# Kernel optimization log

Measured on AMD Instinct MI355X. Metric: run time of the kernel, lower is better.

The kernel has to match this reference:

```python
import jax, jax.numpy as jnp
import numpy as np

B, S, HID = 2, 2048, 4096
NUM_HEADS, NUM_KV_HEADS, HEAD_DIM = 32, 8, 128
KV_SIZE = HID * NUM_KV_HEADS // NUM_HEADS  # 1024


def setup_inputs() -> dict:
    key = jax.random.key(0)
    ks = jax.random.split(key, 5)
    x = jax.random.normal(ks[0], (B, S, HID), dtype=jnp.float32)
    wq = jax.random.normal(ks[1], (HID, HID), dtype=jnp.float32) * 0.02
    wk = jax.random.normal(ks[2], (HID, KV_SIZE), dtype=jnp.float32) * 0.02
    wv = jax.random.normal(ks[3], (HID, KV_SIZE), dtype=jnp.float32) * 0.02
    wo = jax.random.normal(ks[4], (KV_SIZE, HID), dtype=jnp.float32) * 0.02
    return {"x": x, "wq": wq, "wk": wk, "wv": wv, "wo": wo}


def reference(x, wq, wk, wv, wo):
    b, s, _ = x.shape
    g = NUM_HEADS // NUM_KV_HEADS  # num_head_groups
    q = x @ wq  # [b, s, hid]
    k = x @ wk  # [b, s, kv_size]
    v = x @ wv  # [b, s, kv_size]
    # 'b s (h d) -> b h s d' with h = num_heads
    q = q.reshape(b, s, NUM_HEADS, HEAD_DIM).transpose(0, 2, 1, 3)
    # 'b s (h d) -> b h d s' with h = num_kv_heads
    k = k.reshape(b, s, NUM_KV_HEADS, HEAD_DIM).transpose(0, 2, 3, 1)
    # 'b s (h d) -> b h s d'
    v = v.reshape(b, s, NUM_KV_HEADS, HEAD_DIM).transpose(0, 2, 1, 3)
    # 'b (h g) s d -> b g h s d' with g = num_head_groups, h = num_kv_heads
    q = q.reshape(b, NUM_KV_HEADS, g, s, HEAD_DIM).transpose(0, 2, 1, 3, 4)
    # NOTE: faithful to source - g is contracted (summed) here, it does not
    # appear in the output subscripts.
    scores = jnp.einsum('bghqd,bhdk->bhqk', q, k) / jnp.sqrt(
        jnp.asarray(HEAD_DIM, dtype=x.dtype))
    scores = jax.nn.softmax(scores, axis=-1)
    values = jnp.einsum('bhqk,bhkd->bhqd', scores, v)  # [b, h_kv, s, d]
    values = values.transpose(0, 2, 1, 3).reshape(b, s, KV_SIZE)
    return values @ wo  # [b, s, hid]
```

## Files before the change

kernel.cpp:

```cpp
#include <hip/hip_runtime.h>
#include <stdint.h>

#define S 2048
#define HID 4096
#define NKV 8
#define HD 128
#define KV 1024
#define BATCH 2
#define NQKV 3072
#define MROWS 4096

typedef __attribute__((ext_vector_type(4))) float f32x4;
typedef __attribute__((ext_vector_type(8))) __bf16 bf16x8;
typedef __attribute__((ext_vector_type(8))) unsigned short ushort8;
typedef __attribute__((ext_vector_type(4))) unsigned short ushort4_t;
typedef __attribute__((ext_vector_type(4))) float float4_t;

__device__ __forceinline__ unsigned short f2bf(float f) {
    unsigned int u = __builtin_bit_cast(unsigned int, f);
    u += 0x7fffu + ((u >> 16) & 1u);
    return (unsigned short)(u >> 16);
}
__device__ __forceinline__ float bf2f(unsigned short s) {
    unsigned int u = ((unsigned int)s) << 16;
    return __builtin_bit_cast(float, u);
}

__device__ __forceinline__ void gl2lds16(const void* g, void* l) {
    __builtin_amdgcn_global_load_lds(
        (const __attribute__((address_space(1))) void*)(uintptr_t)(g),
        (__attribute__((address_space(3))) void*)(uintptr_t)(l),
        16, 0, 0);
}

__global__ __launch_bounds__(256) void castx_kernel(const float* __restrict__ x,
                                                    unsigned short* __restrict__ xb) {
    int i = (blockIdx.x * 256 + threadIdx.x) * 4;
    float4_t v = *(const float4_t*)&x[i];
    ushort4_t o;
    o.x = f2bf(v.x); o.y = f2bf(v.y); o.z = f2bf(v.z); o.w = f2bf(v.w);
    *(ushort4_t*)&xb[i] = o;
}

__global__ __launch_bounds__(256) void wcat_kernel(const float* __restrict__ wq,
                                                   const float* __restrict__ wk,
                                                   const float* __restrict__ wv,
                                                   unsigned short* __restrict__ WcatT) {
    __shared__ float T[64 * 65];
    const int tid = threadIdx.x;
    const int k0 = blockIdx.x * 64;
    const int n0 = blockIdx.y * 64;
    const float scale = 0.088388347648318447f;
#pragma unroll
    for (int i = 0; i < 16; i++) {
        int kl = (tid >> 6) + i * 4;
        int nl = tid & 63;
        int k = k0 + kl, n = n0 + nl;
        float v;
        if (n < KV) {
            int kvh = n >> 7, d = n & 127;
            const float* p = wq + (size_t)k * HID + kvh * 512 + d;
            v = (p[0] + p[128] + p[256] + p[384]) * scale;
        } else if (n < 2048) {
            v = wk[(size_t)k * KV + (n - KV)];
        } else {
            v = wv[(size_t)k * KV + (n - 2048)];
        }
        T[kl * 65 + nl] = v;
    }
    __syncthreads();
#pragma unroll
    for (int i = 0; i < 16; i++) {
        int nl = (tid >> 6) + i * 4;
        int kl = tid & 63;
        WcatT[(size_t)(n0 + nl) * HID + k0 + kl] = f2bf(T[kl * 65 + nl]);
    }
}

__global__ __launch_bounds__(256) void wot_kernel(const float* __restrict__ wo,
                                                  unsigned short* __restrict__ woT) {
    __shared__ float T[64 * 65];
    const int tid = threadIdx.x;
    const int k0 = blockIdx.x * 64;
    const int n0 = blockIdx.y * 64;
#pragma unroll
    for (int i = 0; i < 16; i++) {
        int kl = (tid >> 6) + i * 4, nl = tid & 63;
        T[kl * 65 + nl] = wo[(size_t)(k0 + kl) * HID + n0 + nl];
    }
    __syncthreads();
#pragma unroll
    for (int i = 0; i < 16; i++) {
        int nl = (tid >> 6) + i * 4, kl = tid & 63;
        woT[(size_t)(n0 + nl) * KV + k0 + kl] = f2bf(T[kl * 65 + nl]);
    }
}

template <int OUT_BF16>
__global__ __launch_bounds__(256) void gemm_bt(const unsigned short* __restrict__ A,
                                               const unsigned short* __restrict__ Bt,
                                               void* __restrict__ Cv,
                                               int M, int N, int K) {
    __shared__ unsigned short Asl[128 * 32];
    __shared__ unsigned short Bsl[128 * 32];
    const int tid = threadIdx.x;
    const int lane = tid & 63;
    const int wave = tid >> 6;
    const int lm = lane & 15;
    const int quad = lane >> 4;
    const int wm = (wave >> 1) << 6;
    const int wn = (wave & 1) << 6;
    const int m0 = blockIdx.y * 128;
    const int n0 = blockIdx.x * 128;

    f32x4 acc[4][4] = {};

    const int r0 = tid >> 2;
    const int kc = tid & 3;
    const int gsw = kc ^ ((r0 >> 1) & 3);
    const int rsw = (lm >> 1) & 3;
    const size_t Abase = (size_t)(m0 + r0) * K + gsw * 8;
    const size_t Bbase = (size_t)(n0 + r0) * K + gsw * 8;
    unsigned short* As0 = &Asl[tid * 8];
    unsigned short* As1 = &Asl[(tid + 256) * 8];
    unsigned short* Bs0 = &Bsl[tid * 8];
    unsigned short* Bs1 = &Bsl[(tid + 256) * 8];

    for (int k0 = 0; k0 < K; k0 += 32) {
        gl2lds16(A + Abase + k0, As0);
        gl2lds16(A + Abase + (size_t)64 * K + k0, As1);
        gl2lds16(Bt + Bbase + k0, Bs0);
        gl2lds16(Bt + Bbase + (size_t)64 * K + k0, Bs1);
        __syncthreads();
        bf16x8 af[4], bfr[4];
#pragma unroll
        for (int i = 0; i < 4; i++)
            af[i] = *(const bf16x8*)&Asl[(wm + i * 16 + lm) * 32 + (quad ^ rsw) * 8];
#pragma unroll
        for (int j = 0; j < 4; j++)
            bfr[j] = *(const bf16x8*)&Bsl[(wn + j * 16 + lm) * 32 + (quad ^ rsw) * 8];
#pragma unroll
        for (int i = 0; i < 4; i++)
#pragma unroll
            for (int j = 0; j < 4; j++)
                acc[i][j] = __builtin_amdgcn_mfma_f32_16x16x32_bf16(af[i], bfr[j], acc[i][j], 0, 0, 0);
        __syncthreads();
    }
#pragma unroll
    for (int i = 0; i < 4; i++) {
        const int row = m0 + wm + i * 16 + quad * 4;
#pragma unroll
        for (int j = 0; j < 4; j++) {
            const int col = n0 + wn + j * 16 + lm;
#pragma unroll
            for (int r = 0; r < 4; r++) {
                if (OUT_BF16)
                    ((unsigned short*)Cv)[(size_t)(row + r) * N + col] = f2bf(acc[i][j][r]);
                else
                    ((float*)Cv)[(size_t)(row + r) * N + col] = acc[i][j][r];
            }
        }
    }
}

__global__ __launch_bounds__(256) void vt_kernel(const unsigned short* __restrict__ QKV,
                                                 unsigned short* __restrict__ Vt) {
    __shared__ unsigned short T[128 * 136];
    const int tid = threadIdx.x;
    const int st = blockIdx.x;
    const int bh = blockIdx.y;
    const int b = bh >> 3, h = bh & 7;
#pragma unroll
    for (int it = 0; it < 8; it++) {
        int chunk = tid + it * 256;
        int s = chunk >> 4, cc = chunk & 15;
        ushort8 v = *(const ushort8*)&QKV[(size_t)(b * S + st * 128 + s) * NQKV + 2048 + h * HD + cc * 8];
        *(ushort8*)&T[s * 136 + cc * 8] = v;
    }
    __syncthreads();
#pragma unroll
    for (int it = 0; it < 8; it++) {
        int chunk = tid + it * 256;
        int d = chunk >> 4, scc = chunk & 15;
        ushort8 o;
#pragma unroll
        for (int j = 0; j < 8; j++) o[j] = T[(scc * 8 + j) * 136 + d];
        *(ushort8*)&Vt[(size_t)((b * NKV + h) * HD + d) * S + st * 128 + scc * 8] = o;
    }
}

__global__ __launch_bounds__(256, 1) void attn_kernel(const unsigned short* __restrict__ QKV,
                                                      const unsigned short* __restrict__ Vt,
                                                      unsigned short* __restrict__ Oout) {
    __shared__ unsigned short Ks[64 * 128];
    __shared__ unsigned short Vs[128 * 64];
    __shared__ unsigned short Ps[128 * 64];
    const int tid = threadIdx.x;
    const int lane = tid & 63, wave = tid >> 6;
    const int lm = lane & 15, quad = lane >> 4;
    const int sw = lm & 7;
    const int qt = blockIdx.x;
    const int h = blockIdx.y;
    const int b = blockIdx.z;
    const int qrow0 = qt * 128 + wave * 32;

    bf16x8 qf[2][4];
#pragma unroll
    for (int rt = 0; rt < 2; rt++)
#pragma unroll
        for (int ks = 0; ks < 4; ks++) {
            size_t off = (size_t)(b * S + qrow0 + rt * 16 + lm) * NQKV + h * HD + ks * 32 + quad * 8;
            qf[rt][ks] = *(const bf16x8*)&QKV[off];
        }

    float lsum[2][4] = {};
    f32x4 oacc[2][8] = {};

    const int krow = tid >> 2, kc4 = tid & 3;
    const int vrow = tid >> 1, vc2 = tid & 1;
    const unsigned short* Kg0 = QKV + (size_t)(b * S) * NQKV + KV + h * HD + kc4 * 32;
    const unsigned short* Vg0 = Vt + (size_t)((b * NKV + h) * HD + vrow) * S + vc2 * 32;

    ushort8 kreg[4], vreg[4];
    {
        const unsigned short* kg = Kg0 + (size_t)krow * NQKV;
        const unsigned short* vg = Vg0;
#pragma unroll
        for (int j = 0; j < 4; j++) kreg[j] = *(const ushort8*)(kg + j * 8);
#pragma unroll
        for (int j = 0; j < 4; j++) vreg[j] = *(const ushort8*)(vg + j * 8);
    }

    for (int kt = 0; kt < 32; kt++) {
        __syncthreads();
#pragma unroll
        for (int j = 0; j < 4; j++)
            *(ushort8*)&Ks[krow * 128 + ((kc4 * 4 + j) ^ (krow & 7)) * 8] = kreg[j];
#pragma unroll
        for (int j = 0; j < 4; j++)
            *(ushort8*)&Vs[vrow * 64 + ((vc2 * 4 + j) ^ (vrow & 7)) * 8] = vreg[j];
        __syncthreads();
        if (kt < 31) {
            const unsigned short* kg = Kg0 + (size_t)((kt + 1) * 64 + krow) * NQKV;
            const unsigned short* vg = Vg0 + (kt + 1) * 64;
#pragma unroll
            for (int j = 0; j < 4; j++) kreg[j] = *(const ushort8*)(kg + j * 8);
#pragma unroll
            for (int j = 0; j < 4; j++) vreg[j] = *(const ushort8*)(vg + j * 8);
        }

        f32x4 sc[2][4] = {};
#pragma unroll
        for (int ks = 0; ks < 4; ks++)
#pragma unroll
            for (int ct = 0; ct < 4; ct++) {
                bf16x8 kf = *(const bf16x8*)&Ks[(ct * 16 + lm) * 128 + ((ks * 4 + quad) ^ sw) * 8];
                sc[0][ct] = __builtin_amdgcn_mfma_f32_16x16x32_bf16(qf[0][ks], kf, sc[0][ct], 0, 0, 0);
                sc[1][ct] = __builtin_amdgcn_mfma_f32_16x16x32_bf16(qf[1][ks], kf, sc[1][ct], 0, 0, 0);
            }

#pragma unroll
        for (int rt = 0; rt < 2; rt++)
#pragma unroll
            for (int ct = 0; ct < 4; ct++)
#pragma unroll
                for (int r = 0; r < 4; r++) {
                    float p = __expf(fminf(sc[rt][ct][r], 60.f));
                    unsigned short pb = f2bf(p);
                    lsum[rt][r] += bf2f(pb);
                    int prow = wave * 32 + rt * 16 + quad * 4 + r;
                    int pcol = ct * 16 + lm;
                    Ps[prow * 64 + (((pcol >> 3) ^ (prow & 7)) * 8) + (pcol & 7)] = pb;
                }

#pragma unroll
        for (int ks = 0; ks < 2; ks++) {
            bf16x8 af0 = *(const bf16x8*)&Ps[(wave * 32 + lm) * 64 + ((ks * 4 + quad) ^ sw) * 8];
            bf16x8 af1 = *(const bf16x8*)&Ps[(wave * 32 + 16 + lm) * 64 + ((ks * 4 + quad) ^ sw) * 8];
#pragma unroll
            for (int dt = 0; dt < 8; dt++) {
                bf16x8 vf = *(const bf16x8*)&Vs[(dt * 16 + lm) * 64 + ((ks * 4 + quad) ^ sw) * 8];
                oacc[0][dt] = __builtin_amdgcn_mfma_f32_16x16x32_bf16(af0, vf, oacc[0][dt], 0, 0, 0);
                oacc[1][dt] = __builtin_amdgcn_mfma_f32_16x16x32_bf16(af1, vf, oacc[1][dt], 0, 0, 0);
            }
        }
    }

#pragma unroll
    for (int rt = 0; rt < 2; rt++)
#pragma unroll
        for (int r = 0; r < 4; r++) {
            float v = lsum[rt][r];
            v += __shfl_xor(v, 8);
            v += __shfl_xor(v, 4);
            v += __shfl_xor(v, 2);
            v += __shfl_xor(v, 1);
            lsum[rt][r] = v;
        }
#pragma unroll
    for (int rt = 0; rt < 2; rt++)
#pragma unroll
        for (int dt = 0; dt < 8; dt++)
#pragma unroll
            for (int r = 0; r < 4; r++) {
                int row = b * S + qt * 128 + wave * 32 + rt * 16 + quad * 4 + r;
                int col = h * HD + dt * 16 + lm;
                Oout[(size_t)row * KV + col] = f2bf(oacc[rt][dt][r] / lsum[rt][r]);
            }
}

extern "C" void kernel_launch(void* const* d_in, const int* in_sizes, int n_in,
                              void* d_out, int out_size, void* d_ws, size_t ws_size,
                              hipStream_t stream) {
    (void)in_sizes; (void)n_in; (void)out_size; (void)ws_size;
    const float* x  = (const float*)d_in[0];
    const float* wq = (const float*)d_in[1];
    const float* wk = (const float*)d_in[2];
    const float* wv = (const float*)d_in[3];
    const float* wo = (const float*)d_in[4];
    float* out = (float*)d_out;
    char* ws = (char*)d_ws;

    unsigned short* xb    = (unsigned short*)(ws);
    unsigned short* WcatT = (unsigned short*)(ws + 33554432);
    unsigned short* woT   = (unsigned short*)(ws + 33554432 + 25165824);
    unsigned short* QKV   = (unsigned short*)(ws + 67108864);
    unsigned short* Vt    = (unsigned short*)(ws);
    unsigned short* AttnO = (unsigned short*)(ws + 8388608);

    castx_kernel<<<16384, 256, 0, stream>>>(x, xb);
    wcat_kernel<<<dim3(64, 48), 256, 0, stream>>>(wq, wk, wv, WcatT);
    wot_kernel<<<dim3(16, 64), 256, 0, stream>>>(wo, woT);
    gemm_bt<1><<<dim3(NQKV / 128, MROWS / 128), 256, 0, stream>>>(xb, WcatT, QKV, MROWS, NQKV, HID);
    vt_kernel<<<dim3(16, 16), 256, 0, stream>>>(QKV, Vt);
    attn_kernel<<<dim3(16, NKV, BATCH), 256, 0, stream>>>(QKV, Vt, AttnO);
    gemm_bt<0><<<dim3(HID / 128, MROWS / 128), 256, 0, stream>>>(AttnO, woT, out, MROWS, HID, KV);
}
```

Baseline: 455.9 us.

## Replace GEMM with 256x256 tiled, double-buffered, 8-wave pipelined kernel

Replaces the simple 128x128 single-buffered bf16 GEMM with a 512-thread kernel that computes 256x256 tiles over 64-wide K steps. Global-to-LDS loads for the next K tile are double-buffered and interleaved with MFMA quarters, separated by barriers and explicit vmcnt waits, with s_setprio raised around the MFMA blocks. It also swizzles the LDS layout and remaps block IDs across 8 groups for better cache locality. The goal is to hide memory latency and raise data reuse, at the cost of much higher LDS and register use (two blocks per CU) and fewer blocks for these matrix sizes.

```diff
diff --git a/kernel.cpp b/kernel.cpp
--- a/kernel.cpp
+++ b/kernel.cpp
@@ -96,71 +96,150 @@
     }
 }
 
+#define BAR() do { asm volatile("" ::: "memory"); __builtin_amdgcn_s_barrier(); asm volatile("" ::: "memory"); } while (0)
+#define WAITV2() asm volatile("s_waitcnt vmcnt(2)" ::: "memory")
+
+__device__ __forceinline__ void stage2(const unsigned short* __restrict__ g,
+                                       size_t so0, size_t so1,
+                                       unsigned short* lds, int tid) {
+    gl2lds16(g + so0, lds + (size_t)tid * 8);
+    gl2lds16(g + so1, lds + (size_t)(512 + tid) * 8);
+}
+
 template <int OUT_BF16>
-__global__ __launch_bounds__(256) void gemm_bt(const unsigned short* __restrict__ A,
-                                               const unsigned short* __restrict__ Bt,
-                                               void* __restrict__ Cv,
-                                               int M, int N, int K) {
-    __shared__ unsigned short Asl[128 * 32];
-    __shared__ unsigned short Bsl[128 * 32];
+__global__ __launch_bounds__(512, 2) void gemm_bt8(const unsigned short* __restrict__ A,
+                                                   const unsigned short* __restrict__ Bt,
+                                                   void* __restrict__ Cv,
+                                                   int M, int N, int K) {
+    __shared__ unsigned short As[2][2][8192];
+    __shared__ unsigned short Bs[2][2][8192];
     const int tid = threadIdx.x;
-    const int lane = tid & 63;
-    const int wave = tid >> 6;
-    const int lm = lane & 15;
-    const int quad = lane >> 4;
-    const int wm = (wave >> 1) << 6;
-    const int wn = (wave & 1) << 6;
-    const int m0 = blockIdx.y * 128;
-    const int n0 = blockIdx.x * 128;
-
-    f32x4 acc[4][4] = {};
-
-    const int r0 = tid >> 2;
-    const int kc = tid & 3;
-    const int gsw = kc ^ ((r0 >> 1) & 3);
-    const int rsw = (lm >> 1) & 3;
-    const size_t Abase = (size_t)(m0 + r0) * K + gsw * 8;
-    const size_t Bbase = (size_t)(n0 + r0) * K + gsw * 8;
-    unsigned short* As0 = &Asl[tid * 8];
-    unsigned short* As1 = &Asl[(tid + 256) * 8];
-    unsigned short* Bs0 = &Bsl[tid * 8];
-    unsigned short* Bs1 = &Bsl[(tid + 256) * 8];
-
-    for (int k0 = 0; k0 < K; k0 += 32) {
-        gl2lds16(A + Abase + k0, As0);
-        gl2lds16(A + Abase + (size_t)64 * K + k0, As1);
-        gl2lds16(Bt + Bbase + k0, Bs0);
-        gl2lds16(Bt + Bbase + (size_t)64 * K + k0, Bs1);
-        __syncthreads();
-        bf16x8 af[4], bfr[4];
-#pragma unroll
-        for (int i = 0; i < 4; i++)
-            af[i] = *(const bf16x8*)&Asl[(wm + i * 16 + lm) * 32 + (quad ^ rsw) * 8];
-#pragma unroll
-        for (int j = 0; j < 4; j++)
-            bfr[j] = *(const bf16x8*)&Bsl[(wn + j * 16 + lm) * 32 + (quad ^ rsw) * 8];
-#pragma unroll
-        for (int i = 0; i < 4; i++)
-#pragma unroll
-            for (int j = 0; j < 4; j++)
-                acc[i][j] = __builtin_amdgcn_mfma_f32_16x16x32_bf16(af[i], bfr[j], acc[i][j], 0, 0, 0);
-        __syncthreads();
-    }
-#pragma unroll
-    for (int i = 0; i < 4; i++) {
-        const int row = m0 + wm + i * 16 + quad * 4;
-#pragma unroll
-        for (int j = 0; j < 4; j++) {
-            const int col = n0 + wn + j * 16 + lm;
+    const int lane = tid & 63, wave = tid >> 6;
+    const int lm = lane & 15, quad = lane >> 4;
+    const int wm = wave >> 2;
+    const int wn = wave & 3;
+    const int wnh = wn >> 1;
+    const int wnb = (wn & 1) * 4;
+
+    const int nbx = gridDim.x;
+    const int id = blockIdx.y * nbx + blockIdx.x;
+    const int cpx = (nbx * gridDim.y) >> 3;
+    const int sid = (id & 7) * cpx + (id >> 3);
+    const int m0 = (sid / nbx) * 256;
+    const int n0 = (sid % nbx) * 256;
+
+    size_t so0, so1;
+    {
+#pragma unroll
+        for (int i = 0; i < 2; i++) {
+            int p = i * 512 + tid;
+            int ps = p ^ (((p >> 5) & 1) << 1);
+            int s = ps >> 6, w = ps & 63;
+            int row = ((s >> 1) << 4) + (w >> 2);
+            int kc = ((s & 1) << 5) + ((w & 3) << 3);
+            size_t off = (size_t)row * K + kc;
+            if (i == 0) so0 = off; else so1 = off;
+        }
+    }
+    const unsigned short* Agb = A + (size_t)m0 * K;
+    const unsigned short* Bgb = Bt + (size_t)n0 * K;
+    const size_t hK = (size_t)128 * K;
+
+    const int roff = lm * 32 + ((quad << 3) ^ (((lm >> 3) & 1) << 4));
+
+#define LDA(mi, kk, BUF) a[(mi) & 3][kk] = *(const bf16x8*)&As[BUF][wm][(((mi) * 2 + (kk)) << 9) + roff]
+#define LDB(ni, kk, BUF) b[ni][kk] = *(const bf16x8*)&Bs[BUF][wnh][(((wnb + (ni)) * 2 + (kk)) << 9) + roff]
+#define RD_A_LO(BUF) { LDA(0,0,BUF); LDA(0,1,BUF); LDA(1,0,BUF); LDA(1,1,BUF); LDA(2,0,BUF); LDA(2,1,BUF); LDA(3,0,BUF); LDA(3,1,BUF); }
+#define RD_A_HI(BUF) { LDA(4,0,BUF); LDA(4,1,BUF); LDA(5,0,BUF); LDA(5,1,BUF); LDA(6,0,BUF); LDA(6,1,BUF); LDA(7,0,BUF); LDA(7,1,BUF); }
+#define RD_B_LO(BUF) { LDB(0,0,BUF); LDB(0,1,BUF); LDB(1,0,BUF); LDB(1,1,BUF); }
+#define RD_B_HI(BUF) { LDB(2,0,BUF); LDB(2,1,BUF); LDB(3,0,BUF); LDB(3,1,BUF); }
+#define MFMA_Q(MB, NB) do { \
+    __builtin_amdgcn_s_setprio(1); \
+    _Pragma("unroll") for (int i_ = 0; i_ < 4; i_++) \
+    _Pragma("unroll") for (int j_ = 0; j_ < 2; j_++) \
+    _Pragma("unroll") for (int k_ = 0; k_ < 2; k_++) \
+        acc[(MB) + i_][(NB) + j_] = __builtin_amdgcn_mfma_f32_16x16x32_bf16( \
+            a[i_][k_], b[(NB) + j_][k_], acc[(MB) + i_][(NB) + j_], 0, 0, 0); \
+    __builtin_amdgcn_s_setprio(0); \
+} while (0)
+
+    f32x4 acc[8][4] = {};
+    bf16x8 a[4][2], b[4][2];
+
+    const int KT = K >> 6;
+    const int NT = KT >> 1;
+
+    stage2(Agb, so0, so1, &As[0][0][0], tid);
+    stage2(Agb + hK, so0, so1, &As[0][1][0], tid);
+    stage2(Bgb, so0, so1, &Bs[0][0][0], tid);
+    stage2(Bgb + hK, so0, so1, &Bs[0][1][0], tid);
+    stage2(Agb + 64, so0, so1, &As[1][0][0], tid);
+    WAITV2();
+    BAR();
+
+    for (int t = 0; t < NT; ++t) {
+        const int t1 = 2 * t + 1;
+        int t2 = 2 * t + 2; if (t2 >= KT) t2 = KT - 1;
+        int t3 = 2 * t + 3; if (t3 >= KT) t3 = KT - 1;
+        const size_t k1 = (size_t)t1 * 64, k2 = (size_t)t2 * 64, k3 = (size_t)t3 * 64;
+
+        RD_A_LO(0); RD_B_LO(0);
+        stage2(Agb + hK + k1, so0, so1, &As[1][1][0], tid);
+        BAR(); MFMA_Q(0, 0); BAR();
+
+        RD_B_HI(0);
+        stage2(Bgb + k1, so0, so1, &Bs[1][0][0], tid);
+        BAR(); MFMA_Q(0, 2); BAR();
+
+        RD_A_HI(0);
+        stage2(Bgb + hK + k1, so0, so1, &Bs[1][1][0], tid);
+        BAR(); MFMA_Q(4, 2); BAR();
+
+        stage2(Agb + k2, so0, so1, &As[0][0][0], tid);
+        BAR(); MFMA_Q(4, 0);
+        WAITV2();
+        BAR();
+
+        RD_A_LO(1); RD_B_LO(1);
+        stage2(Agb + hK + k2, so0, so1, &As[0][1][0], tid);
+        BAR(); MFMA_Q(0, 0); BAR();
+
+        RD_B_HI(1);
+        stage2(Bgb + k2, so0, so1, &Bs[0][0][0], tid);
+        BAR(); MFMA_Q(0, 2); BAR();
+
+        RD_A_HI(1);
+        stage2(Bgb + hK + k2, so0, so1, &Bs[0][1][0], tid);
+        BAR(); MFMA_Q(4, 2); BAR();
+
+        stage2(Agb + k3, so0, so1, &As[1][0][0], tid);
+        BAR(); MFMA_Q(4, 0);
+        WAITV2();
+        BAR();
+    }
+
+    const int crow0 = m0 + wm * 128 + quad * 4;
+    const int ccol0 = n0 + wn * 64 + lm;
+#pragma unroll
+    for (int mi = 0; mi < 8; mi++)
+#pragma unroll
+        for (int ni = 0; ni < 4; ni++)
 #pragma unroll
             for (int r = 0; r < 4; r++) {
+                const int row = crow0 + mi * 16 + r;
+                const int col = ccol0 + ni * 16;
                 if (OUT_BF16)
-                    ((unsigned short*)Cv)[(size_t)(row + r) * N + col] = f2bf(acc[i][j][r]);
+                    ((unsigned short*)Cv)[(size_t)row * N + col] = f2bf(acc[mi][ni][r]);
                 else
-                    ((float*)Cv)[(size_t)(row + r) * N + col] = acc[i][j][r];
+                    ((float*)Cv)[(size_t)row * N + col] = acc[mi][ni][r];
             }
-        }
-    }
+#undef LDA
+#undef LDB
+#undef RD_A_LO
+#undef RD_A_HI
+#undef RD_B_LO
+#undef RD_B_HI
+#undef MFMA_Q
 }
 
 __global__ __launch_bounds__(256) void vt_kernel(const unsigned short* __restrict__ QKV,
@@ -331,8 +410,8 @@
     castx_kernel<<<16384, 256, 0, stream>>>(x, xb);
     wcat_kernel<<<dim3(64, 48), 256, 0, stream>>>(wq, wk, wv, WcatT);
     wot_kernel<<<dim3(16, 64), 256, 0, stream>>>(wo, woT);
-    gemm_bt<1><<<dim3(NQKV / 128, MROWS / 128), 256, 0, stream>>>(xb, WcatT, QKV, MROWS, NQKV, HID);
+    gemm_bt8<1><<<dim3(NQKV / 256, MROWS / 256), 512, 0, stream>>>(xb, WcatT, QKV, MROWS, NQKV, HID);
     vt_kernel<<<dim3(16, 16), 256, 0, stream>>>(QKV, Vt);
     attn_kernel<<<dim3(16, NKV, BATCH), 256, 0, stream>>>(QKV, Vt, AttnO);
-    gemm_bt<0><<<dim3(HID / 128, MROWS / 128), 256, 0, stream>>>(AttnO, woT, out, MROWS, HID, KV);
-}
+    gemm_bt8<0><<<dim3(HID / 256, MROWS / 256), 512, 0, stream>>>(AttnO, woT, out, MROWS, HID, KV);
+}
```

After: 426.3 us. -6.5%, faster.
